# Performance work log

Hardware: AMD Instinct MI355X
Metric: run time of the kernel (lower is better)

## Reference

```python
import jax, jax.numpy as jnp
import numpy as np

ALPHA = 0.9     # projection strength
EPS = 1e-3      # Lyapunov positive-definite regularizer (lyapunov_eps)
B, D, H = 32768, 512, 64


def setup_inputs() -> dict:
    key = jax.random.key(0)
    ks = jax.random.split(key, 8)
    def w(k, shape, fan_in):
        return jax.random.normal(k, shape, jnp.float32) * (1.0 / fan_in) ** 0.5
    return dict(
        x=jax.random.normal(ks[0], (B, D), jnp.float32),
        # dynamics MLP f(x): D -> 64 -> 64 -> D
        W1=w(ks[1], (D, H), D), b1=jnp.zeros((H,), jnp.float32),
        W2=w(ks[2], (H, H), H), b2=jnp.zeros((H,), jnp.float32),
        W3=w(ks[3], (H, D), H), b3=jnp.zeros((D,), jnp.float32),
        # Lyapunov MLP V(z): D -> 64 -> 64 -> 1 (+ eps*||z||^2)
        V1=w(ks[4], (D, H), D), c1=jnp.zeros((H,), jnp.float32),
        V2=w(ks[5], (H, H), H), c2=jnp.zeros((H,), jnp.float32),
        V3=w(ks[6], (H, 1), H), c3=jnp.zeros((1,), jnp.float32),
    )


def reference(x, W1, b1, W2, b2, W3, b3, V1, c1, V2, c2, V3, c3):
    def fnet(xx):  # nominal dynamics: [B,D] -> [B,D]
        h = jax.nn.relu(xx @ W1 + b1)
        h = jax.nn.relu(h @ W2 + b2)
        return h @ W3 + b3

    def vnet(z):  # Lyapunov candidate: [B,D] -> [B]
        h = jax.nn.relu(z @ V1 + c1)
        h = jax.nn.relu(h @ V2 + c2)
        return (h @ V3 + c3)[..., 0] + EPS * jnp.sum(z * z, axis=-1)

    def lyap_sum(xx):
        v = vnet(fnet(xx))
        return jnp.sum(v), v

    # grad_v replicates the in-forward lyapunov.backward(...): dV(f(x))/dx, shape [B,D]
    (_, lyap), grad_v = jax.value_and_grad(lyap_sum, has_aux=True)(x)

    f = fnet(x)                                   # [B, D]
    dot = jnp.sum(grad_v * grad_v, axis=-1)       # bmm(gv, fv): per-sample <grad_v, grad_v>
    denom = jnp.sum(grad_v * grad_v)              # global .pow(2).sum() over all elements
    orth = jax.nn.relu(dot + ALPHA * lyap) / denom  # [B]
    return f - orth[:, None] * grad_v             # diag_embed(orth) @ grad_v
```

## Files before the change

### kernel.cpp

```cpp
#include <hip/hip_runtime.h>

#define ALPHA_C 0.9f
#define EPS_C 1e-3f

typedef unsigned short u16;
typedef __attribute__((ext_vector_type(8))) short short8;
typedef __attribute__((ext_vector_type(4))) short short4v;
typedef __attribute__((ext_vector_type(4))) float f32x4;
#define MFMA(a, b, c) __builtin_amdgcn_mfma_f32_16x16x32_bf16(a, b, c, 0, 0, 0)
#define LDS_FENCE() asm volatile("" ::: "memory")
#define BAR_TOP()    { LDS_FENCE(); __builtin_amdgcn_s_barrier(); LDS_FENCE(); }
#define BAR_STAGED() { LDS_FENCE(); asm volatile("s_waitcnt lgkmcnt(0)" ::: "memory"); \
                       __builtin_amdgcn_s_barrier(); LDS_FENCE(); }

__device__ __forceinline__ u16 f2bf(float f) {
  union { float f; unsigned u; } v; v.f = f;
  unsigned u = v.u;
  u += 0x7FFFu + ((u >> 16) & 1u);
  return (u16)(u >> 16);
}
__device__ __forceinline__ float bf2f(u16 h) {
  union { unsigned u; float f; } v; v.u = ((unsigned)h) << 16;
  return v.f;
}

__global__ __launch_bounds__(256) void k_conv(
    const float* __restrict__ W1, const float* __restrict__ W2, const float* __restrict__ W3,
    const float* __restrict__ V1, const float* __restrict__ V2,
    u16* __restrict__ PW1T, u16* __restrict__ PW1n, u16* __restrict__ PV1T, u16* __restrict__ PV1n,
    u16* __restrict__ PW3T, u16* __restrict__ PW3n, u16* __restrict__ PW2T, u16* __restrict__ PW2n,
    u16* __restrict__ PV2T, u16* __restrict__ PV2n, float* __restrict__ DP) {
  int i = blockIdx.x * 256 + threadIdx.x;
  if (i < 256) DP[i] = 0.f;
  {
    int k = i >> 6, j = i & 63;
    u16 b = f2bf(W1[i]);
    PW1T[((((j >> 4) * 16 + (k >> 5)) * 4 + ((k & 31) >> 3)) * 16 + (j & 15)) * 8 + (k & 7)] = b;
    PW1n[((((k >> 4) * 2 + (j >> 5)) * 4 + ((j & 31) >> 3)) * 16 + (k & 15)) * 8 + (j & 7)] = b;
    u16 c = f2bf(V1[i]);
    PV1T[((((j >> 4) * 16 + (k >> 5)) * 4 + ((k & 31) >> 3)) * 16 + (j & 15)) * 8 + (k & 7)] = c;
    PV1n[((((k >> 4) * 2 + (j >> 5)) * 4 + ((j & 31) >> 3)) * 16 + (k & 15)) * 8 + (j & 7)] = c;
  }
  {
    int k = i >> 9, n = i & 511;
    u16 b = f2bf(W3[i]);
    PW3T[((((n >> 4) * 2 + (k >> 5)) * 4 + ((k & 31) >> 3)) * 16 + (n & 15)) * 8 + (k & 7)] = b;
    PW3n[((((k >> 4) * 16 + (n >> 5)) * 4 + ((n & 31) >> 3)) * 16 + (k & 15)) * 8 + (n & 7)] = b;
  }
  if (i < 4096) {
    int k = i >> 6, j = i & 63;
    u16 b = f2bf(W2[i]);
    PW2T[((((j >> 4) * 2 + (k >> 5)) * 4 + ((k & 31) >> 3)) * 16 + (j & 15)) * 8 + (k & 7)] = b;
    PW2n[((((k >> 4) * 2 + (j >> 5)) * 4 + ((j & 31) >> 3)) * 16 + (k & 15)) * 8 + (j & 7)] = b;
    u16 c = f2bf(V2[i]);
    PV2T[((((j >> 4) * 2 + (k >> 5)) * 4 + ((k & 31) >> 3)) * 16 + (j & 15)) * 8 + (k & 7)] = c;
    PV2n[((((k >> 4) * 2 + (j >> 5)) * 4 + ((j & 31) >> 3)) * 16 + (k & 15)) * 8 + (j & 7)] = c;
  }
}

#define LDG8(dst, P, FRAG)                                                      \
  _Pragma("unroll") for (int j = 0; j < 8; ++j)                                 \
    dst[j] = *(const short8*)&P[((size_t)(FRAG) * 64 + lane) * 8];

#define STAGE16B(DST, P, SRCFRAG)                                               \
  _Pragma("unroll") for (int c = 0; c < 2; ++c)                                 \
    *(short8*)&Ws[((DST) * 512) + (c * 512 + tid) * 8] =                        \
      *(const short8*)&P[((size_t)(SRCFRAG) * 512) + (c * 512 + tid) * 8];

#define STAGE4x4B(DST, P, OFF)                                                  \
  _Pragma("unroll") for (int c = 0; c < 2; ++c) {                               \
    int t_ = c * 2 + (tid >> 8);                                                \
    *(short8*)&Ws[((DST) + t_ * 4) * 512 + (tid & 255) * 8] =                   \
      *(const short8*)&P[((size_t)(t_ * 16 + (OFF))) * 512 + (tid & 255) * 8];  \
  }

__global__ __launch_bounds__(512, 4) void k_fused(
    const float* __restrict__ x,
    const u16* __restrict__ PW1T, const float* __restrict__ b1,
    const u16* __restrict__ PW2T, const float* __restrict__ b2,
    const u16* __restrict__ PW3T, const float* __restrict__ b3,
    const u16* __restrict__ PV1T, const float* __restrict__ c1,
    const u16* __restrict__ PV2T, const u16* __restrict__ PV2n, const float* __restrict__ c2,
    const float* __restrict__ V3, const float* __restrict__ c3,
    const u16* __restrict__ PV1n, const u16* __restrict__ PW3n,
    const u16* __restrict__ PW2n, const u16* __restrict__ PW1n,
    u16* __restrict__ FP, u16* __restrict__ T2P, u16* __restrict__ GVB,
    float* __restrict__ NUM, float* __restrict__ DP) {
  __shared__ __align__(16) u16 H1s[64 * 72];
  __shared__ __align__(16) u16 H2s[64 * 72];
  __shared__ __align__(16) u16 S2s[64 * 72];
  __shared__ __align__(16) u16 As[64 * 136];
  __shared__ __align__(16) u16 Ws[16384];
  __shared__ float dred[4];
  const int tid = threadIdx.x;
  const int lane = tid & 63, w = tid >> 6, q = lane >> 4, r = lane & 15;
  const int ws = w & 3, wh = w >> 2;
  const int m0 = blockIdx.x * 64;
  const int arow = ws * 16 + r;
  const int strip = blockIdx.x * 4 + ws;
  float* xf = (float*)As;

  f32x4 acc1[2] = {};
  {
    const int L = (wh << 6) | lane, h4 = L >> 5, cc = L & 31;
    const float* xb = x + (size_t)(m0 + ws * 16) * 512;
    float4 xr[4];
    #pragma unroll
    for (int it = 0; it < 4; ++it)
      xr[it] = *(const float4*)&xb[(it * 4 + h4) * 512 + cc * 4];
    #pragma unroll 1
    for (int kc = 0; kc < 4; ++kc) {
      BAR_TOP();
      STAGE4x4B(0, PW1T, kc * 4);
      #pragma unroll
      for (int it = 0; it < 4; ++it) {
        float4 v = xr[it]; short4v s4;
        s4[0] = (short)f2bf(v.x); s4[1] = (short)f2bf(v.y);
        s4[2] = (short)f2bf(v.z); s4[3] = (short)f2bf(v.w);
        *(short4v*)&As[(ws * 16 + it * 4 + h4) * 136 + cc * 4] = s4;
      }
      if (kc < 3) {
        #pragma unroll
        for (int it = 0; it < 4; ++it)
          xr[it] = *(const float4*)&xb[(it * 4 + h4) * 512 + (kc + 1) * 128 + cc * 4];
      }
      BAR_STAGED();
      #pragma unroll
      for (int ks = 0; ks < 4; ++ks) {
        short8 a = *(const short8*)&As[arow * 136 + ks * 32 + q * 8];
        #pragma unroll
        for (int tt = 0; tt < 2; ++tt) {
          short8 b = *(const short8*)&Ws[(((wh * 2 + tt) * 4 + ks) * 64 + lane) * 8];
          acc1[tt] = MFMA(a, b, acc1[tt]);
        }
      }
    }
  }
  #pragma unroll
  for (int tt = 0; tt < 2; ++tt) {
    int col = (wh * 2 + tt) * 16 + r; float bv = b1[col];
    #pragma unroll
    for (int g = 0; g < 4; ++g) {
      float hh = acc1[tt][g] + bv; hh = hh > 0.f ? hh : 0.f;
      H1s[(ws * 16 + q * 4 + g) * 72 + col] = f2bf(hh);
    }
  }
  BAR_STAGED();

  {
    short8 a0 = *(const short8*)&H1s[arow * 72 + 0 + q * 8];
    short8 a1 = *(const short8*)&H1s[arow * 72 + 32 + q * 8];
    f32x4 acc2[2] = {};
    #pragma unroll
    for (int tt = 0; tt < 2; ++tt) {
      int t = wh * 2 + tt;
      short8 b0 = *(const short8*)&PW2T[((t * 2 + 0) * 64 + lane) * 8];
      short8 b1 = *(const short8*)&PW2T[((t * 2 + 1) * 64 + lane) * 8];
      acc2[tt] = MFMA(a0, b0, acc2[tt]);
      acc2[tt] = MFMA(a1, b1, acc2[tt]);
    }
    #pragma unroll
    for (int tt = 0; tt < 2; ++tt) {
      int col = (wh * 2 + tt) * 16 + r; float bv = b2[col];
      #pragma unroll
      for (int g = 0; g < 4; ++g) {
        float hh = acc2[tt][g] + bv; hh = hh > 0.f ? hh : 0.f;
        H2s[(ws * 16 + q * 4 + g) * 72 + col] = f2bf(hh);
      }
    }
  }
  BAR_STAGED();
  short8 h2a0 = *(const short8*)&H2s[arow * 72 + 0 + q * 8];
  short8 h2a1 = *(const short8*)&H2s[arow * 72 + 32 + q * 8];

  f32x4 g1acc[2] = {};
  float ssqp[4] = {0.f, 0.f, 0.f, 0.f};
  #pragma unroll 1
  for (int nc = 0; nc < 4; ++nc) {
    BAR_TOP();
    STAGE16B(0, PW3T, nc * 16);
    STAGE4x4B(16, PV1T, nc * 4);
    BAR_STAGED();
    f32x4 facc[4] = {};
    #pragma unroll
    for (int tt = 0; tt < 4; ++tt) {
      int t = wh * 4 + tt;
      short8 b0 = *(const short8*)&Ws[((t * 2 + 0) * 64 + lane) * 8];
      short8 b1 = *(const short8*)&Ws[((t * 2 + 1) * 64 + lane) * 8];
      facc[tt] = MFMA(h2a0, b0, facc[tt]);
      facc[tt] = MFMA(h2a1, b1, facc[tt]);
    }
    #pragma unroll
    for (int tt = 0; tt < 4; ++tt) {
      int t = wh * 4 + tt;
      float bv = b3[nc * 128 + t * 16 + r];
      short4v s4;
      #pragma unroll
      for (int g = 0; g < 4; ++g) {
        float v = facc[tt][g] + bv;
        ssqp[g] += v * v;
        u16 bb = f2bf(v);
        As[(ws * 16 + q * 4 + g) * 136 + t * 16 + r] = bb;
        s4[g] = (short)bb;
      }
      *(short4v*)&FP[(size_t)(((strip * 4 + nc) * 8 + t) * 64 + lane) * 4] = s4;
    }
    BAR_STAGED();
    #pragma unroll
    for (int ks = 0; ks < 4; ++ks) {
      short8 a = *(const short8*)&As[arow * 136 + ks * 32 + q * 8];
      #pragma unroll
      for (int tt = 0; tt < 2; ++tt) {
        int t = wh * 2 + tt;
        short8 b = *(const short8*)&Ws[((16 + t * 4 + ks) * 64 + lane) * 8];
        g1acc[tt] = MFMA(a, b, g1acc[tt]);
      }
    }
  }

  f32x4 g1v[2];
  #pragma unroll
  for (int tt = 0; tt < 2; ++tt) {
    int col = (wh * 2 + tt) * 16 + r; float cv = c1[col];
    #pragma unroll
    for (int g = 0; g < 4; ++g) {
      float v = g1acc[tt][g] + cv; v = v > 0.f ? v : 0.f;
      g1v[tt][g] = v;
      S2s[(ws * 16 + q * 4 + g) * 72 + col] = f2bf(v);
    }
  }
  BAR_STAGED();
  f32x4 g2acc[2] = {};
  {
    short8 a0 = *(const short8*)&S2s[arow * 72 + 0 + q * 8];
    short8 a1 = *(const short8*)&S2s[arow * 72 + 32 + q * 8];
    #pragma unroll
    for (int tt = 0; tt < 2; ++tt) {
      int t = wh * 2 + tt;
      short8 b0 = *(const short8*)&PV2T[((t * 2 + 0) * 64 + lane) * 8];
      short8 b1 = *(const short8*)&PV2T[((t * 2 + 1) * 64 + lane) * 8];
      g2acc[tt] = MFMA(a0, b0, g2acc[tt]);
      g2acc[tt] = MFMA(a1, b1, g2acc[tt]);
    }
  }
  float totp[4] = {0.f, 0.f, 0.f, 0.f};
  #pragma unroll
  for (int tt = 0; tt < 2; ++tt) {
    int col = (wh * 2 + tt) * 16 + r;
    float c2v = c2[col], v3v = V3[col];
    #pragma unroll
    for (int g = 0; g < 4; ++g) {
      float pre = g2acc[tt][g] + c2v;
      float g2 = pre > 0.f ? pre : 0.f;
      S2s[(ws * 16 + q * 4 + g) * 72 + col] = pre > 0.f ? f2bf(v3v) : (u16)0;
      totp[g] += g2 * v3v;
    }
  }
  BAR_STAGED();
  f32x4 s2acc[2] = {};
  {
    short8 a0 = *(const short8*)&S2s[arow * 72 + 0 + q * 8];
    short8 a1 = *(const short8*)&S2s[arow * 72 + 32 + q * 8];
    #pragma unroll
    for (int tt = 0; tt < 2; ++tt) {
      int t = wh * 2 + tt;
      short8 b0 = *(const short8*)&PV2n[((t * 2 + 0) * 64 + lane) * 8];
      short8 b1 = *(const short8*)&PV2n[((t * 2 + 1) * 64 + lane) * 8];
      s2acc[tt] = MFMA(a0, b0, s2acc[tt]);
      s2acc[tt] = MFMA(a1, b1, s2acc[tt]);
    }
  }
  #pragma unroll
  for (int tt = 0; tt < 2; ++tt) {
    int col = (wh * 2 + tt) * 16 + r;
    #pragma unroll
    for (int g = 0; g < 4; ++g) {
      float sv = g1v[tt][g] > 0.f ? s2acc[tt][g] : 0.f;
      S2s[(ws * 16 + q * 4 + g) * 72 + col] = f2bf(sv);
    }
  }
  BAR_STAGED();
  #pragma unroll
  for (int g = 0; g < 4; ++g) {
    float s = totp[g] + EPS_C * ssqp[g];
    s += __shfl_xor(s, 1); s += __shfl_xor(s, 2); s += __shfl_xor(s, 4); s += __shfl_xor(s, 8);
    if (r == 0) xf[w * 16 + q * 4 + g] = s;
  }
  BAR_STAGED();
  float c3v = c3[0];
  float lyap_row[4];
  #pragma unroll
  for (int g = 0; g < 4; ++g)
    lyap_row[g] = xf[w * 16 + q * 4 + g] + xf[(w ^ 4) * 16 + q * 4 + g] + c3v;

  asm volatile("s_waitcnt vmcnt(0)" ::: "memory");

  f32x4 t3acc[2] = {};
  short8 s2a0 = *(const short8*)&S2s[arow * 72 + 0 + q * 8];
  short8 s2a1 = *(const short8*)&S2s[arow * 72 + 32 + q * 8];
  #pragma unroll 1
  for (int nc = 0; nc < 4; ++nc) {
    BAR_TOP();
    STAGE16B(0, PV1n, nc * 16);
    STAGE4x4B(16, PW3n, nc * 4);
    BAR_STAGED();
    short4v fpr[4];
    #pragma unroll
    for (int tt = 0; tt < 4; ++tt)
      fpr[tt] = *(const short4v*)&FP[(size_t)(((strip * 4 + nc) * 8 + wh * 4 + tt) * 64 + lane) * 4];
    f32x4 uacc[4] = {};
    #pragma unroll
    for (int tt = 0; tt < 4; ++tt) {
      int t = wh * 4 + tt;
      short8 b0 = *(const short8*)&Ws[((t * 2 + 0) * 64 + lane) * 8];
      short8 b1 = *(const short8*)&Ws[((t * 2 + 1) * 64 + lane) * 8];
      uacc[tt] = MFMA(s2a0, b0, uacc[tt]);
      uacc[tt] = MFMA(s2a1, b1, uacc[tt]);
    }
    #pragma unroll
    for (int tt = 0; tt < 4; ++tt) {
      int t = wh * 4 + tt;
      #pragma unroll
      for (int g = 0; g < 4; ++g) {
        As[(ws * 16 + q * 4 + g) * 136 + t * 16 + r] =
            f2bf(uacc[tt][g] + 2.f * EPS_C * bf2f((u16)fpr[tt][g]));
      }
    }
    BAR_STAGED();
    #pragma unroll
    for (int ks = 0; ks < 4; ++ks) {
      short8 a = *(const short8*)&As[arow * 136 + ks * 32 + q * 8];
      #pragma unroll
      for (int tt = 0; tt < 2; ++tt) {
        int t = wh * 2 + tt;
        short8 b = *(const short8*)&Ws[((16 + t * 4 + ks) * 64 + lane) * 8];
        t3acc[tt] = MFMA(a, b, t3acc[tt]);
      }
    }
  }
  #pragma unroll
  for (int tt = 0; tt < 2; ++tt) {
    int col = (wh * 2 + tt) * 16 + r;
    #pragma unroll
    for (int g = 0; g < 4; ++g) {
      int addr = (ws * 16 + q * 4 + g) * 72 + col;
      u16 h2 = H2s[addr];
      H2s[addr] = h2 ? f2bf(t3acc[tt][g]) : (u16)0;
    }
  }
  BAR_STAGED();
  f32x4 t2acc[2] = {};
  {
    short8 a0 = *(const short8*)&H2s[arow * 72 + 0 + q * 8];
    short8 a1 = *(const short8*)&H2s[arow * 72 + 32 + q * 8];
    #pragma unroll
    for (int tt = 0; tt < 2; ++tt) {
      int t = wh * 2 + tt;
      short8 b0 = *(const short8*)&PW2n[((t * 2 + 0) * 64 + lane) * 8];
      short8 b1 = *(const short8*)&PW2n[((t * 2 + 1) * 64 + lane) * 8];
      t2acc[tt] = MFMA(a0, b0, t2acc[tt]);
      t2acc[tt] = MFMA(a1, b1, t2acc[tt]);
    }
  }
  #pragma unroll
  for (int tt = 0; tt < 2; ++tt) {
    int col = (wh * 2 + tt) * 16 + r;
    #pragma unroll
    for (int g = 0; g < 4; ++g) {
      int addr = (ws * 16 + q * 4 + g) * 72 + col;
      u16 h1 = H1s[addr];
      H1s[addr] = h1 ? f2bf(t2acc[tt][g]) : (u16)0;
    }
  }
  BAR_STAGED();
  short8 v0 = *(const short8*)&H1s[arow * 72 + 0 + q * 8];
  short8 v1 = *(const short8*)&H1s[arow * 72 + 32 + q * 8];
  if (wh == 0) *(short8*)&T2P[(size_t)((strip * 2 + 0) * 64 + lane) * 8] = v0;
  else         *(short8*)&T2P[(size_t)((strip * 2 + 1) * 64 + lane) * 8] = v1;

  float ssq2p[4] = {0.f, 0.f, 0.f, 0.f};
  #pragma unroll 1
  for (int nc = 0; nc < 4; ++nc) {
    BAR_TOP();
    STAGE16B(0, PW1n, nc * 16);
    BAR_STAGED();
    #pragma unroll
    for (int tt = 0; tt < 4; ++tt) {
      int t = wh * 4 + tt;
      short8 b0 = *(const short8*)&Ws[((t * 2 + 0) * 64 + lane) * 8];
      short8 b1 = *(const short8*)&Ws[((t * 2 + 1) * 64 + lane) * 8];
      f32x4 a = {};
      a = MFMA(v0, b0, a);
      a = MFMA(v1, b1, a);
      short4v s4;
      #pragma unroll
      for (int g = 0; g < 4; ++g) {
        ssq2p[g] += a[g] * a[g];
        s4[g] = (short)f2bf(a[g]);
      }
      if (GVB != nullptr)
        *(short4v*)&GVB[(size_t)(((strip * 4 + nc) * 8 + t) * 64 + lane) * 4] = s4;
    }
  }
  #pragma unroll
  for (int g = 0; g < 4; ++g) {
    float s = ssq2p[g];
    s += __shfl_xor(s, 1); s += __shfl_xor(s, 2); s += __shfl_xor(s, 4); s += __shfl_xor(s, 8);
    if (r == 0) xf[w * 16 + q * 4 + g] = s;
  }
  BAR_STAGED();
  float totw = 0.f;
  #pragma unroll
  for (int g = 0; g < 4; ++g) {
    float s = xf[w * 16 + q * 4 + g] + xf[(w ^ 4) * 16 + q * 4 + g];
    if (r == 0 && wh == 0) {
      int rowg = m0 + ws * 16 + q * 4 + g;
      float nm = s + ALPHA_C * lyap_row[g];
      NUM[rowg] = nm > 0.f ? nm : 0.f;
    }
    s += __shfl_xor(s, 16); s += __shfl_xor(s, 32);
    totw += s;
  }
  if (lane == 0 && wh == 0) dred[ws] = totw;
  __syncthreads();
  if (tid == 0) atomicAdd(&DP[blockIdx.x & 255], dred[0] + dred[1] + dred[2] + dred[3]);
}

__global__ __launch_bounds__(256, 2) void k_out(
    const u16* __restrict__ T2P, const u16* __restrict__ PW1n,
    const u16* __restrict__ FP, const float* __restrict__ NUM, const float* __restrict__ DP,
    float* __restrict__ out) {
  __shared__ float red[256];
  __shared__ __align__(16) float OutS[64 * 132];
  const int tid = threadIdx.x;
  const int lane = tid & 63, w = tid >> 6, q = lane >> 4, r = lane & 15;
  const int m0 = blockIdx.x * 64;
  const int strip = blockIdx.x * 4 + w;
  red[tid] = DP[tid];
  __syncthreads();
  for (int s = 128; s >= 1; s >>= 1) {
    if (tid < s) red[tid] += red[tid + s];
    __syncthreads();
  }
  const float inv_denom = 1.f / red[0];
  float sc[4];
  #pragma unroll
  for (int g = 0; g < 4; ++g) sc[g] = NUM[m0 + w * 16 + q * 4 + g] * inv_denom;
  short8 a0 = *(const short8*)&T2P[(size_t)((strip * 2 + 0) * 64 + lane) * 8];
  short8 a1 = *(const short8*)&T2P[(size_t)((strip * 2 + 1) * 64 + lane) * 8];
  short8 bA[8], bB[8];
  LDG8(bA, PW1n, ((j >> 1) * 2 + (j & 1)));
  #pragma unroll 1
  for (int nc = 0; nc < 4; ++nc) {
    LDG8(bB, PW1n, ((nc * 8 + 4 + (j >> 1)) * 2 + (j & 1)));
    short4v fpr[8];
    #pragma unroll
    for (int t = 0; t < 8; ++t)
      fpr[t] = *(const short4v*)&FP[(size_t)(((strip * 4 + nc) * 8 + t) * 64 + lane) * 4];
    f32x4 acc[8] = {};
    #pragma unroll
    for (int t = 0; t < 4; ++t) {
      acc[t] = MFMA(a0, bA[t * 2 + 0], acc[t]);
      acc[t] = MFMA(a1, bA[t * 2 + 1], acc[t]);
    }
    int ncn = (nc + 1) & 3;
    LDG8(bA, PW1n, ((ncn * 8 + (j >> 1)) * 2 + (j & 1)));
    #pragma unroll
    for (int t = 0; t < 4; ++t) {
      acc[4 + t] = MFMA(a0, bB[t * 2 + 0], acc[4 + t]);
      acc[4 + t] = MFMA(a1, bB[t * 2 + 1], acc[4 + t]);
    }
    #pragma unroll
    for (int t = 0; t < 8; ++t) {
      #pragma unroll
      for (int g = 0; g < 4; ++g)
        OutS[(w * 16 + q * 4 + g) * 132 + t * 16 + r] =
            bf2f((u16)fpr[t][g]) - sc[g] * acc[t][g];
    }
    LDS_FENCE();
    #pragma unroll
    for (int jj = 0; jj < 8; ++jj) {
      f32x4 ov = *(const f32x4*)&OutS[(w * 16 + (lane >> 5) + jj * 2) * 132 + (lane & 31) * 4];
      *(f32x4*)&out[(size_t)(m0 + w * 16 + (lane >> 5) + jj * 2) * 512 + nc * 128 + (lane & 31) * 4] = ov;
    }
    LDS_FENCE();
  }
}

__global__ __launch_bounds__(256, 2) void k_out2(
    const u16* __restrict__ FP, const u16* __restrict__ GVB,
    const float* __restrict__ NUM, const float* __restrict__ DP,
    float* __restrict__ out) {
  __shared__ float red[256];
  __shared__ __align__(16) float OutS[64 * 132];
  const int tid = threadIdx.x;
  const int lane = tid & 63, w = tid >> 6, q = lane >> 4, r = lane & 15;
  const int m0 = blockIdx.x * 64;
  const int strip = blockIdx.x * 4 + w;
  const int h = lane >> 5, c4 = lane & 31;
  red[tid] = DP[tid];
  __syncthreads();
  for (int s = 128; s >= 1; s >>= 1) {
    if (tid < s) red[tid] += red[tid + s];
    __syncthreads();
  }
  const float inv_denom = 1.f / red[0];
  float sc[4];
  #pragma unroll
  for (int g = 0; g < 4; ++g) sc[g] = NUM[m0 + w * 16 + q * 4 + g] * inv_denom;
  #pragma unroll 1
  for (int nc = 0; nc < 4; ++nc) {
    #pragma unroll
    for (int t = 0; t < 8; ++t) {
      size_t base = (size_t)(((strip * 4 + nc) * 8 + t) * 64 + lane) * 4;
      short4v f4 = *(const short4v*)&FP[base];
      short4v g4 = *(const short4v*)&GVB[base];
      #pragma unroll
      for (int g = 0; g < 4; ++g)
        OutS[(w * 16 + q * 4 + g) * 132 + t * 16 + r] =
            bf2f((u16)f4[g]) - sc[g] * bf2f((u16)g4[g]);
    }
    LDS_FENCE();
    #pragma unroll
    for (int jj = 0; jj < 8; ++jj) {
      f32x4 ov = *(const f32x4*)&OutS[(w * 16 + h + jj * 2) * 132 + c4 * 4];
      *(f32x4*)&out[(size_t)(m0 + w * 16 + h + jj * 2) * 512 + nc * 128 + c4 * 4] = ov;
    }
    LDS_FENCE();
  }
}

extern "C" void kernel_launch(void* const* d_in, const int* in_sizes, int n_in,
                              void* d_out, int out_size, void* d_ws, size_t ws_size,
                              hipStream_t stream) {
  const float* x  = (const float*)d_in[0];
  const float* W1 = (const float*)d_in[1];
  const float* b1 = (const float*)d_in[2];
  const float* W2 = (const float*)d_in[3];
  const float* b2 = (const float*)d_in[4];
  const float* W3 = (const float*)d_in[5];
  const float* b3 = (const float*)d_in[6];
  const float* V1 = (const float*)d_in[7];
  const float* c1 = (const float*)d_in[8];
  const float* V2 = (const float*)d_in[9];
  const float* c2 = (const float*)d_in[10];
  const float* V3 = (const float*)d_in[11];
  const float* c3 = (const float*)d_in[12];
  float* out = (float*)d_out;

  u16* FP  = (u16*)d_ws;
  u16* T2P = FP + 16777216;
  float* NUM = (float*)(T2P + 2097152);
  float* DP  = NUM + 32768;
  u16* PW1T = (u16*)(DP + 256);
  u16* PW1n = PW1T + 32768;
  u16* PV1T = PW1n + 32768;
  u16* PV1n = PV1T + 32768;
  u16* PW3T = PV1n + 32768;
  u16* PW3n = PW3T + 32768;
  u16* PW2T = PW3n + 32768;
  u16* PW2n = PW2T + 4096;
  u16* PV2T = PW2n + 4096;
  u16* PV2n = PV2T + 4096;
  u16* GVB_base = PV2n + 4096;
  size_t need_bytes = ((size_t)(GVB_base - (u16*)d_ws) + 16777216) * sizeof(u16);
  u16* GVB = (ws_size >= need_bytes) ? GVB_base : nullptr;

  k_conv<<<128, 256, 0, stream>>>(W1, W2, W3, V1, V2,
                                  PW1T, PW1n, PV1T, PV1n, PW3T, PW3n,
                                  PW2T, PW2n, PV2T, PV2n, DP);
  k_fused<<<512, 512, 0, stream>>>(x, PW1T, b1, PW2T, b2, PW3T, b3, PV1T, c1,
                                   PV2T, PV2n, c2, V3, c3, PV1n, PW3n, PW2n, PW1n,
                                   FP, T2P, GVB, NUM, DP);
  if (GVB != nullptr) {
    k_out2<<<512, 256, 0, stream>>>(FP, GVB, NUM, DP, out);
  } else {
    k_out<<<512, 256, 0, stream>>>(T2P, PW1n, FP, NUM, DP, out);
  }
}
```

Before: 175.2 us.

## Register-prefetch next weight chunks before LDS staging, stagger half the blocks

```diff
diff --git a/kernel.cpp b/kernel.cpp
--- a/kernel.cpp
+++ b/kernel.cpp
@@ -62,17 +62,20 @@
   _Pragma("unroll") for (int j = 0; j < 8; ++j)                                 \
     dst[j] = *(const short8*)&P[((size_t)(FRAG) * 64 + lane) * 8];
 
-#define STAGE16B(DST, P, SRCFRAG)                                               \
-  _Pragma("unroll") for (int c = 0; c < 2; ++c)                                 \
-    *(short8*)&Ws[((DST) * 512) + (c * 512 + tid) * 8] =                        \
-      *(const short8*)&P[((size_t)(SRCFRAG) * 512) + (c * 512 + tid) * 8];
-
-#define STAGE4x4B(DST, P, OFF)                                                  \
-  _Pragma("unroll") for (int c = 0; c < 2; ++c) {                               \
-    int t_ = c * 2 + (tid >> 8);                                                \
-    *(short8*)&Ws[((DST) + t_ * 4) * 512 + (tid & 255) * 8] =                   \
-      *(const short8*)&P[((size_t)(t_ * 16 + (OFF))) * 512 + (tid & 255) * 8];  \
-  }
+#define LD16Q(R0, R1, P, SRCFRAG) {                                             \
+  R0 = *(const short8*)&P[((size_t)(SRCFRAG) * 512) + (0 * 512 + tid) * 8];     \
+  R1 = *(const short8*)&P[((size_t)(SRCFRAG) * 512) + (1 * 512 + tid) * 8]; }
+#define WR16Q(DST, R0, R1) {                                                    \
+  *(short8*)&Ws[((DST) * 512) + (0 * 512 + tid) * 8] = R0;                      \
+  *(short8*)&Ws[((DST) * 512) + (1 * 512 + tid) * 8] = R1; }
+#define LD4x4Q(R0, R1, P, OFF) {                                                \
+  int t0_ = (tid >> 8), t1_ = 2 + (tid >> 8);                                   \
+  R0 = *(const short8*)&P[((size_t)(t0_ * 16 + (OFF))) * 512 + (tid & 255) * 8];\
+  R1 = *(const short8*)&P[((size_t)(t1_ * 16 + (OFF))) * 512 + (tid & 255) * 8]; }
+#define WR4x4Q(DST, R0, R1) {                                                   \
+  int t0_ = (tid >> 8), t1_ = 2 + (tid >> 8);                                   \
+  *(short8*)&Ws[((DST) + t0_ * 4) * 512 + (tid & 255) * 8] = R0;                \
+  *(short8*)&Ws[((DST) + t1_ * 4) * 512 + (tid & 255) * 8] = R1; }
 
 __global__ __launch_bounds__(512, 4) void k_fused(
     const float* __restrict__ x,
@@ -100,6 +103,8 @@
   const int strip = blockIdx.x * 4 + ws;
   float* xf = (float*)As;
 
+  if (blockIdx.x & 256) { __builtin_amdgcn_s_sleep(64); }
+
   f32x4 acc1[2] = {};
   {
     const int L = (wh << 6) | lane, h4 = L >> 5, cc = L & 31;
@@ -108,10 +113,12 @@
     #pragma unroll
     for (int it = 0; it < 4; ++it)
       xr[it] = *(const float4*)&xb[(it * 4 + h4) * 512 + cc * 4];
+    short8 pw0, pw1;
+    LD4x4Q(pw0, pw1, PW1T, 0);
     #pragma unroll 1
     for (int kc = 0; kc < 4; ++kc) {
       BAR_TOP();
-      STAGE4x4B(0, PW1T, kc * 4);
+      WR4x4Q(0, pw0, pw1);
       #pragma unroll
       for (int it = 0; it < 4; ++it) {
         float4 v = xr[it]; short4v s4;
@@ -123,6 +130,7 @@
         #pragma unroll
         for (int it = 0; it < 4; ++it)
           xr[it] = *(const float4*)&xb[(it * 4 + h4) * 512 + (kc + 1) * 128 + cc * 4];
+        LD4x4Q(pw0, pw1, PW1T, (kc + 1) * 4);
       }
       BAR_STAGED();
       #pragma unroll
@@ -175,45 +183,54 @@
 
   f32x4 g1acc[2] = {};
   float ssqp[4] = {0.f, 0.f, 0.f, 0.f};
-  #pragma unroll 1
-  for (int nc = 0; nc < 4; ++nc) {
-    BAR_TOP();
-    STAGE16B(0, PW3T, nc * 16);
-    STAGE4x4B(16, PV1T, nc * 4);
-    BAR_STAGED();
-    f32x4 facc[4] = {};
-    #pragma unroll
-    for (int tt = 0; tt < 4; ++tt) {
-      int t = wh * 4 + tt;
-      short8 b0 = *(const short8*)&Ws[((t * 2 + 0) * 64 + lane) * 8];
-      short8 b1 = *(const short8*)&Ws[((t * 2 + 1) * 64 + lane) * 8];
-      facc[tt] = MFMA(h2a0, b0, facc[tt]);
-      facc[tt] = MFMA(h2a1, b1, facc[tt]);
-    }
-    #pragma unroll
-    for (int tt = 0; tt < 4; ++tt) {
-      int t = wh * 4 + tt;
-      float bv = b3[nc * 128 + t * 16 + r];
-      short4v s4;
-      #pragma unroll
-      for (int g = 0; g < 4; ++g) {
-        float v = facc[tt][g] + bv;
-        ssqp[g] += v * v;
-        u16 bb = f2bf(v);
-        As[(ws * 16 + q * 4 + g) * 136 + t * 16 + r] = bb;
-        s4[g] = (short)bb;
-      }
-      *(short4v*)&FP[(size_t)(((strip * 4 + nc) * 8 + t) * 64 + lane) * 4] = s4;
-    }
-    BAR_STAGED();
-    #pragma unroll
-    for (int ks = 0; ks < 4; ++ks) {
-      short8 a = *(const short8*)&As[arow * 136 + ks * 32 + q * 8];
-      #pragma unroll
-      for (int tt = 0; tt < 2; ++tt) {
-        int t = wh * 2 + tt;
-        short8 b = *(const short8*)&Ws[((16 + t * 4 + ks) * 64 + lane) * 8];
-        g1acc[tt] = MFMA(a, b, g1acc[tt]);
+  {
+    short8 bw0, bw1, bv0, bv1;
+    LD16Q(bw0, bw1, PW3T, 0);
+    LD4x4Q(bv0, bv1, PV1T, 0);
+    #pragma unroll 1
+    for (int nc = 0; nc < 4; ++nc) {
+      BAR_TOP();
+      WR16Q(0, bw0, bw1);
+      WR4x4Q(16, bv0, bv1);
+      if (nc < 3) {
+        LD16Q(bw0, bw1, PW3T, (nc + 1) * 16);
+        LD4x4Q(bv0, bv1, PV1T, (nc + 1) * 4);
+      }
+      BAR_STAGED();
+      f32x4 facc[4] = {};
+      #pragma unroll
+      for (int tt = 0; tt < 4; ++tt) {
+        int t = wh * 4 + tt;
+        short8 b0 = *(const short8*)&Ws[((t * 2 + 0) * 64 + lane) * 8];
+        short8 b1 = *(const short8*)&Ws[((t * 2 + 1) * 64 + lane) * 8];
+        facc[tt] = MFMA(h2a0, b0, facc[tt]);
+        facc[tt] = MFMA(h2a1, b1, facc[tt]);
+      }
+      #pragma unroll
+      for (int tt = 0; tt < 4; ++tt) {
+        int t = wh * 4 + tt;
+        float bv = b3[nc * 128 + t * 16 + r];
+        short4v s4;
+        #pragma unroll
+        for (int g = 0; g < 4; ++g) {
+          float v = facc[tt][g] + bv;
+          ssqp[g] += v * v;
+          u16 bb = f2bf(v);
+          As[(ws * 16 + q * 4 + g) * 136 + t * 16 + r] = bb;
+          s4[g] = (short)bb;
+        }
+        *(short4v*)&FP[(size_t)(((strip * 4 + nc) * 8 + t) * 64 + lane) * 4] = s4;
+      }
+      BAR_STAGED();
+      #pragma unroll
+      for (int ks = 0; ks < 4; ++ks) {
+        short8 a = *(const short8*)&As[arow * 136 + ks * 32 + q * 8];
+        #pragma unroll
+        for (int tt = 0; tt < 2; ++tt) {
+          int t = wh * 2 + tt;
+          short8 b = *(const short8*)&Ws[((16 + t * 4 + ks) * 64 + lane) * 8];
+          g1acc[tt] = MFMA(a, b, g1acc[tt]);
+        }
       }
     }
   }
@@ -280,6 +297,9 @@
     }
   }
   BAR_STAGED();
+  short8 cw0, cw1, cv0, cv1;
+  LD16Q(cw0, cw1, PV1n, 0);
+  LD4x4Q(cv0, cv1, PW3n, 0);
   #pragma unroll
   for (int g = 0; g < 4; ++g) {
     float s = totp[g] + EPS_C * ssqp[g];
@@ -301,13 +321,17 @@
   #pragma unroll 1
   for (int nc = 0; nc < 4; ++nc) {
     BAR_TOP();
-    STAGE16B(0, PV1n, nc * 16);
-    STAGE4x4B(16, PW3n, nc * 4);
-    BAR_STAGED();
+    WR16Q(0, cw0, cw1);
+    WR4x4Q(16, cv0, cv1);
+    if (nc < 3) {
+      LD16Q(cw0, cw1, PV1n, (nc + 1) * 16);
+      LD4x4Q(cv0, cv1, PW3n, (nc + 1) * 4);
+    }
     short4v fpr[4];
     #pragma unroll
     for (int tt = 0; tt < 4; ++tt)
       fpr[tt] = *(const short4v*)&FP[(size_t)(((strip * 4 + nc) * 8 + wh * 4 + tt) * 64 + lane) * 4];
+    BAR_STAGED();
     f32x4 uacc[4] = {};
     #pragma unroll
     for (int tt = 0; tt < 4; ++tt) {
@@ -372,6 +396,8 @@
       H1s[addr] = h1 ? f2bf(t2acc[tt][g]) : (u16)0;
     }
   }
+  short8 gw0, gw1;
+  LD16Q(gw0, gw1, PW1n, 0);
   BAR_STAGED();
   short8 v0 = *(const short8*)&H1s[arow * 72 + 0 + q * 8];
   short8 v1 = *(const short8*)&H1s[arow * 72 + 32 + q * 8];
@@ -382,7 +408,8 @@
   #pragma unroll 1
   for (int nc = 0; nc < 4; ++nc) {
     BAR_TOP();
-    STAGE16B(0, PW1n, nc * 16);
+    WR16Q(0, gw0, gw1);
+    if (nc < 3) { LD16Q(gw0, gw1, PW1n, (nc + 1) * 16); }
     BAR_STAGED();
     #pragma unroll
     for (int tt = 0; tt < 4; ++tt) {
```

Result: no change. 176.8 us (+0.9%).
